# Kernel optimization log

Hardware: AMD Instinct MI355X
Metric: run time of the kernel (lower is better)

The kernel has to match this reference:

```python
import jax, jax.numpy as jnp
import numpy as np

N_NODES = 50000

def setup_inputs() -> dict:
    key = jax.random.key(0)
    k1, k2, k3, k4, k5 = jax.random.split(key, 5)
    E, F_IN, F_OUT = 1600000, 48, 48
    edge_feats = jax.random.normal(k1, (E, F_IN), dtype=jnp.float32)
    src = jax.random.randint(k2, (E,), 0, N_NODES, dtype=jnp.int64)
    dst = jax.random.randint(k3, (E,), 0, N_NODES, dtype=jnp.int64)
    # nn.Linear(in_feats, out_feats): weight [out, in], bias [out]
    lim = 1.0 / np.sqrt(F_IN)
    W = jax.random.uniform(k4, (F_OUT, F_IN), minval=-lim, maxval=lim, dtype=jnp.float32)
    b = jax.random.uniform(k5, (F_OUT,), minval=-lim, maxval=lim, dtype=jnp.float32)
    return {"edge_feats": edge_feats, "src": src, "dst": dst, "W": W, "b": b}

def reference(edge_feats, src, dst, W, b):
    # Step 1 (per-node loop in original): node h = mean of in-edge features
    deg = jax.ops.segment_sum(jnp.ones((edge_feats.shape[0],), edge_feats.dtype), dst, num_segments=N_NODES)
    node_h = jax.ops.segment_sum(edge_feats, dst, num_segments=N_NODES) / jnp.maximum(deg, 1.0)[:, None]
    # Step 2 (send/recv): node h' = sum over in-edges of src node h
    h2 = jax.ops.segment_sum(node_h[src], dst, num_segments=N_NODES)
    # Step 3 (edge_list loop): edge h = mean(h'[src], h'[dst])
    edge_h = 0.5 * (h2[src] + h2[dst])
    # Final linear on edge features
    return edge_h @ W.T + b
```

## Files before the change

### kernel.cpp

```cpp
#include <hip/hip_runtime.h>


constexpr int NN = 50000;
constexpr int F  = 48;
constexpr int F4 = F / 4;

typedef float    f32x4 __attribute__((ext_vector_type(4)));
typedef _Float16 f16x4 __attribute__((ext_vector_type(4)));

__global__ void k_zero(int* __restrict__ p, int n) {
    int i = blockIdx.x * blockDim.x + threadIdx.x;
    if (i < n) p[i] = 0;
}

__global__ void k_count(const int4* __restrict__ dst4, int* __restrict__ cnt, int E4) {
    int i = blockIdx.x * blockDim.x + threadIdx.x;
    if (i >= E4) return;
    int4 d = dst4[i];
    atomicAdd(&cnt[d.x], 1);
    atomicAdd(&cnt[d.y], 1);
    atomicAdd(&cnt[d.z], 1);
    atomicAdd(&cnt[d.w], 1);
}

__global__ __launch_bounds__(1024) void k_scan(
    const int4* __restrict__ cnt4, int4* __restrict__ rowptr4,
    int4* __restrict__ cursor4, int* __restrict__ rowptr, int n4, int n)
{
    __shared__ int wsum[16];
    __shared__ int carry_s;
    int t = threadIdx.x;
    int lane = t & 63, wid = t >> 6;
    if (t == 0) carry_s = 0;
    __syncthreads();
    for (int base = 0; base < n4; base += 1024) {
        int c0 = carry_s;
        int i4 = base + t;
        int4 v = (i4 < n4) ? cnt4[i4] : make_int4(0, 0, 0, 0);
        int tsum = v.x + v.y + v.z + v.w;
        int incl = tsum;
#pragma unroll
        for (int d = 1; d < 64; d <<= 1) {
            int u = __shfl_up(incl, d, 64);
            if (lane >= d) incl += u;
        }
        if (lane == 63) wsum[wid] = incl;
        __syncthreads();
        if (wid == 0) {
            int w = (lane < 16) ? wsum[lane] : 0;
            int wincl = w;
#pragma unroll
            for (int d = 1; d < 16; d <<= 1) {
                int u = __shfl_up(wincl, d, 64);
                if (lane >= d) wincl += u;
            }
            if (lane < 16) wsum[lane] = wincl - w;
        }
        __syncthreads();
        int excl = c0 + wsum[wid] + (incl - tsum);
        if (i4 < n4) {
            int p0 = excl, p1 = p0 + v.x, p2 = p1 + v.y, p3 = p2 + v.z;
            int4 r = make_int4(p0, p1, p2, p3);
            rowptr4[i4] = r;
            cursor4[i4] = r;
        }
        __syncthreads();
        if (t == 1023) carry_s = excl + tsum;
        __syncthreads();
    }
    if (t == 0) rowptr[n] = carry_s;
}

__global__ void k_fill(const int4* __restrict__ src4, const int4* __restrict__ dst4,
                       int* __restrict__ cursor, int2* __restrict__ csr_es, int E4) {
    int i = blockIdx.x * blockDim.x + threadIdx.x;
    if (i >= E4) return;
    int4 s = src4[i];
    int4 d = dst4[i];
    int e = i * 4;
    int p0 = atomicAdd(&cursor[d.x], 1);
    int p1 = atomicAdd(&cursor[d.y], 1);
    int p2 = atomicAdd(&cursor[d.z], 1);
    int p3 = atomicAdd(&cursor[d.w], 1);
    csr_es[p0] = make_int2(e + 0, s.x);
    csr_es[p1] = make_int2(e + 1, s.y);
    csr_es[p2] = make_int2(e + 2, s.z);
    csr_es[p3] = make_int2(e + 3, s.w);
}

__global__ __launch_bounds__(256) void k_node_h(
    const f32x4* __restrict__ ef4, const int2* __restrict__ csr_es,
    const int* __restrict__ rowptr, f16x4* __restrict__ nh16, int total)
{
    int idx = blockIdx.x * blockDim.x + threadIdx.x;
    if (idx >= total) return;
    int n = idx / F4;
    int q = idx - n * F4;
    int lo = rowptr[n], hi = rowptr[n + 1];
    f32x4 acc = (f32x4)(0.f);
    int j = lo;
    for (; j + 8 <= hi; j += 8) {
        int e0 = csr_es[j].x,     e1 = csr_es[j + 1].x;
        int e2 = csr_es[j + 2].x, e3 = csr_es[j + 3].x;
        int e4 = csr_es[j + 4].x, e5 = csr_es[j + 5].x;
        int e6 = csr_es[j + 6].x, e7 = csr_es[j + 7].x;
        f32x4 a0 = __builtin_nontemporal_load(&ef4[e0 * F4 + q]);
        f32x4 a1 = __builtin_nontemporal_load(&ef4[e1 * F4 + q]);
        f32x4 a2 = __builtin_nontemporal_load(&ef4[e2 * F4 + q]);
        f32x4 a3 = __builtin_nontemporal_load(&ef4[e3 * F4 + q]);
        f32x4 a4 = __builtin_nontemporal_load(&ef4[e4 * F4 + q]);
        f32x4 a5 = __builtin_nontemporal_load(&ef4[e5 * F4 + q]);
        f32x4 a6 = __builtin_nontemporal_load(&ef4[e6 * F4 + q]);
        f32x4 a7 = __builtin_nontemporal_load(&ef4[e7 * F4 + q]);
        acc += a0 + a1 + a2 + a3 + a4 + a5 + a6 + a7;
    }
    for (; j < hi; j++)
        acc += __builtin_nontemporal_load(&ef4[csr_es[j].x * F4 + q]);
    float inv = 1.0f / fmaxf((float)(hi - lo), 1.0f);
    acc *= inv;
    nh16[idx] = __builtin_convertvector(acc, f16x4);
}

__global__ __launch_bounds__(192) void k_h2lin(
    const f16x4* __restrict__ nh16, const int2* __restrict__ csr_es,
    const int* __restrict__ rowptr, const float* __restrict__ W,
    const float* __restrict__ b, f16x4* __restrict__ h2W16)
{
    __shared__ float h2s[16][F + 1];
    int t = threadIdx.x;
    int nl = t / F4, q = t - nl * F4;
    int node = blockIdx.x * 16 + nl;

    int lo = rowptr[node], hi = rowptr[node + 1];
    f32x4 acc = (f32x4)(0.f);
    int j = lo;
    for (; j + 4 <= hi; j += 4) {
        int s0 = csr_es[j].y,     s1 = csr_es[j + 1].y;
        int s2 = csr_es[j + 2].y, s3 = csr_es[j + 3].y;
        f32x4 a0 = __builtin_convertvector(nh16[s0 * F4 + q], f32x4);
        f32x4 a1 = __builtin_convertvector(nh16[s1 * F4 + q], f32x4);
        f32x4 a2 = __builtin_convertvector(nh16[s2 * F4 + q], f32x4);
        f32x4 a3 = __builtin_convertvector(nh16[s3 * F4 + q], f32x4);
        acc += a0 + a1 + a2 + a3;
    }
    for (; j < hi; j++)
        acc += __builtin_convertvector(nh16[csr_es[j].y * F4 + q], f32x4);

    h2s[nl][q * 4 + 0] = acc.x;
    h2s[nl][q * 4 + 1] = acc.y;
    h2s[nl][q * 4 + 2] = acc.z;
    h2s[nl][q * 4 + 3] = acc.w;
    __syncthreads();

    const float* row = h2s[nl];
    const float* W0 = W + (q * 4 + 0) * F;
    const float* W1 = W + (q * 4 + 1) * F;
    const float* W2 = W + (q * 4 + 2) * F;
    const float* W3 = W + (q * 4 + 3) * F;
    float o0 = 0.f, o1 = 0.f, o2 = 0.f, o3 = 0.f;
#pragma unroll
    for (int i = 0; i < F; i++) {
        float hv = row[i];
        o0 += hv * W0[i];
        o1 += hv * W1[i];
        o2 += hv * W2[i];
        o3 += hv * W3[i];
    }
    const f32x4* b4 = (const f32x4*)b;
    f32x4 r; r.x = o0; r.y = o1; r.z = o2; r.w = o3;
    r = 0.5f * r + 0.5f * b4[q];
    h2W16[node * F4 + q] = __builtin_convertvector(r, f16x4);
}

__global__ void k_edge_out(const int* __restrict__ src, const int* __restrict__ dst,
                           const f16x4* __restrict__ h2W16, f32x4* __restrict__ out4,
                           int total) {
    int idx = blockIdx.x * blockDim.x + threadIdx.x;
    if (idx >= total) return;
    int e = idx / F4;
    int q = idx - e * F4;
    f32x4 x = __builtin_convertvector(h2W16[src[e] * F4 + q], f32x4);
    f32x4 y = __builtin_convertvector(h2W16[dst[e] * F4 + q], f32x4);
    f32x4 r = x + y;
    __builtin_nontemporal_store(r, &out4[idx]);
}

extern "C" void kernel_launch(void* const* d_in, const int* in_sizes, int n_in,
                              void* d_out, int out_size, void* d_ws, size_t ws_size,
                              hipStream_t stream) {
    const float* ef  = (const float*)d_in[0];
    const int*   src = (const int*)d_in[1];
    const int*   dst = (const int*)d_in[2];
    const float* W   = (const float*)d_in[3];
    const float* b   = (const float*)d_in[4];
    float* out = (float*)d_out;
    const int E = in_sizes[1];

    _Float16* nh16  = (_Float16*)d_ws;
    _Float16* h2W16 = nh16 + NN * F;
    int2* csr_es    = (int2*)(h2W16 + NN * F);
    int* rowptr     = (int*)(csr_es + E);
    int* cursor     = rowptr + 50016;
    int* cnt        = cursor + 50016;

    const int totN4 = NN * F4;
    const int totE4 = E * F4;
    const int n4 = NN / 4;
    const int E4 = (E + 3) / 4;

    k_zero<<<(NN + 255) / 256, 256, 0, stream>>>(cnt, NN);
    k_count<<<(E4 + 255) / 256, 256, 0, stream>>>((const int4*)dst, cnt, E4);
    k_scan<<<1, 1024, 0, stream>>>((const int4*)cnt, (int4*)rowptr, (int4*)cursor,
                                   rowptr, n4, NN);
    k_fill<<<(E4 + 255) / 256, 256, 0, stream>>>(
        (const int4*)src, (const int4*)dst, cursor, csr_es, E4);
    k_node_h<<<(totN4 + 255) / 256, 256, 0, stream>>>(
        (const f32x4*)ef, csr_es, rowptr, (f16x4*)nh16, totN4);
    k_h2lin<<<NN / 16, 192, 0, stream>>>(
        (const f16x4*)nh16, csr_es, rowptr, W, b, (f16x4*)h2W16);
    k_edge_out<<<(totE4 + 255) / 256, 256, 0, stream>>>(
        src, dst, (const f16x4*)h2W16, (f32x4*)out, totE4);
}
```

Baseline: 464.0 us.

## Fuse all graph stages into one cooperative persistent kernel with grid syncs

Replaces the seven separate kernel launches with a single cooperative persistent kernel that runs each stage as a grid-stride loop separated by grid.sync. The single-block scan becomes a two-level scan spread across the grid. The h2/linear stage is split into an fp32 aggregation pass and a per-thread matvec that reads the full row from global memory instead of shared memory. The aim is to remove launch gaps and the serial single-block scan, at the cost of grid-wide barriers, a capped grid size (up to 1024 blocks) for the large edge loops, and extra global traffic for the new h2f buffer. The old multi-kernel path is kept as a fallback.

```diff
diff --git a/kernel.cpp b/kernel.cpp
--- a/kernel.cpp
+++ b/kernel.cpp
@@ -1,12 +1,208 @@
 #include <hip/hip_runtime.h>
-
-
-constexpr int NN = 50000;
-constexpr int F  = 48;
-constexpr int F4 = F / 4;
+#include <hip/hip_cooperative_groups.h>
+
+namespace cg = cooperative_groups;
+
+
+constexpr int NN   = 50000;
+constexpr int F    = 48;
+constexpr int F4   = F / 4;
+constexpr int NTHR = 256;
 
 typedef float    f32x4 __attribute__((ext_vector_type(4)));
 typedef _Float16 f16x4 __attribute__((ext_vector_type(4)));
+
+__global__ __launch_bounds__(NTHR, 4) void k_fused(
+    const f32x4* __restrict__ ef4,
+    const int4*  __restrict__ src4, const int4* __restrict__ dst4,
+    const int*   __restrict__ srcs, const int*  __restrict__ dsts,
+    const float* __restrict__ W,    const float* __restrict__ b,
+    f32x4* __restrict__ out4,
+    f16x4* __restrict__ nh16, f16x4* __restrict__ h2W16,
+    f32x4* __restrict__ h2f,
+    int2* __restrict__ csr_es, int* __restrict__ rowptr,
+    int* __restrict__ cursor,  int* __restrict__ cnt,
+    int* __restrict__ wavesum, int E)
+{
+    __shared__ int lws[4];
+    __shared__ int lwe[4];
+    cg::grid_group grid = cg::this_grid();
+
+    const int tid = blockIdx.x * NTHR + threadIdx.x;
+    const int NT  = gridDim.x * NTHR;
+    const int E4  = E >> 2;
+    const int totN4 = NN * F4;
+    const long totE4 = (long)E * F4;
+
+    for (int i = tid; i < NN; i += NT) cnt[i] = 0;
+    __threadfence();
+    grid.sync();
+
+    for (int i = tid; i < E4; i += NT) {
+        int4 d = dst4[i];
+        atomicAdd(&cnt[d.x], 1);
+        atomicAdd(&cnt[d.y], 1);
+        atomicAdd(&cnt[d.z], 1);
+        atomicAdd(&cnt[d.w], 1);
+    }
+    __threadfence();
+    grid.sync();
+
+    const int n4 = NN / 4;
+    const int gwid = tid >> 6, lane = tid & 63;
+    int4 v = make_int4(0, 0, 0, 0);
+    int tsum = 0, incl = 0;
+    if (tid < ((n4 + 63) & ~63)) {
+        if (tid < n4) {
+            v = ((const int4*)cnt)[tid];
+            tsum = v.x + v.y + v.z + v.w;
+        }
+        incl = tsum;
+#pragma unroll
+        for (int d = 1; d < 64; d <<= 1) {
+            int u = __shfl_up(incl, d, 64);
+            if (lane >= d) incl += u;
+        }
+        if (lane == 63) wavesum[gwid] = incl;
+    }
+    __threadfence();
+    grid.sync();
+
+    if (blockIdx.x == 0) {
+        int t = threadIdx.x;
+        int w = (t < 196) ? wavesum[t] : 0;
+        int wl = t & 63, wwid = t >> 6;
+        int winc = w;
+#pragma unroll
+        for (int d = 1; d < 64; d <<= 1) {
+            int u = __shfl_up(winc, d, 64);
+            if (wl >= d) winc += u;
+        }
+        if (wl == 63) lws[wwid] = winc;
+        __syncthreads();
+        if (t == 0) {
+            int run = 0;
+#pragma unroll
+            for (int k = 0; k < 4; k++) { lwe[k] = run; run += lws[k]; }
+            rowptr[NN] = E;
+        }
+        __syncthreads();
+        if (t < 196) wavesum[t] = lwe[wwid] + (winc - w);
+        __threadfence();
+    }
+    grid.sync();
+
+    if (tid < n4) {
+        int base = wavesum[gwid] + (incl - tsum);
+        int4 r;
+        r.x = base; r.y = base + v.x; r.z = r.y + v.y; r.w = r.z + v.z;
+        ((int4*)rowptr)[tid] = r;
+        ((int4*)cursor)[tid] = r;
+    }
+    __threadfence();
+    grid.sync();
+
+    for (int i = tid; i < E4; i += NT) {
+        int4 s = src4[i];
+        int4 d = dst4[i];
+        int e = i * 4;
+        int p0 = atomicAdd(&cursor[d.x], 1);
+        int p1 = atomicAdd(&cursor[d.y], 1);
+        int p2 = atomicAdd(&cursor[d.z], 1);
+        int p3 = atomicAdd(&cursor[d.w], 1);
+        csr_es[p0] = make_int2(e + 0, s.x);
+        csr_es[p1] = make_int2(e + 1, s.y);
+        csr_es[p2] = make_int2(e + 2, s.z);
+        csr_es[p3] = make_int2(e + 3, s.w);
+    }
+    __threadfence();
+    grid.sync();
+
+    for (int idx = tid; idx < totN4; idx += NT) {
+        int n = idx / F4, q = idx - n * F4;
+        int lo = rowptr[n], hi = rowptr[n + 1];
+        f32x4 acc = (f32x4)(0.f);
+        int j = lo;
+        for (; j + 8 <= hi; j += 8) {
+            int e0 = csr_es[j].x,     e1 = csr_es[j + 1].x;
+            int e2 = csr_es[j + 2].x, e3 = csr_es[j + 3].x;
+            int e4 = csr_es[j + 4].x, e5 = csr_es[j + 5].x;
+            int e6 = csr_es[j + 6].x, e7 = csr_es[j + 7].x;
+            f32x4 a0 = __builtin_nontemporal_load(&ef4[e0 * F4 + q]);
+            f32x4 a1 = __builtin_nontemporal_load(&ef4[e1 * F4 + q]);
+            f32x4 a2 = __builtin_nontemporal_load(&ef4[e2 * F4 + q]);
+            f32x4 a3 = __builtin_nontemporal_load(&ef4[e3 * F4 + q]);
+            f32x4 a4 = __builtin_nontemporal_load(&ef4[e4 * F4 + q]);
+            f32x4 a5 = __builtin_nontemporal_load(&ef4[e5 * F4 + q]);
+            f32x4 a6 = __builtin_nontemporal_load(&ef4[e6 * F4 + q]);
+            f32x4 a7 = __builtin_nontemporal_load(&ef4[e7 * F4 + q]);
+            acc += a0 + a1 + a2 + a3 + a4 + a5 + a6 + a7;
+        }
+        for (; j < hi; j++)
+            acc += __builtin_nontemporal_load(&ef4[csr_es[j].x * F4 + q]);
+        float inv = 1.0f / fmaxf((float)(hi - lo), 1.0f);
+        acc *= inv;
+        nh16[idx] = __builtin_convertvector(acc, f16x4);
+    }
+    __threadfence();
+    grid.sync();
+
+    for (int idx = tid; idx < totN4; idx += NT) {
+        int n = idx / F4, q = idx - n * F4;
+        int lo = rowptr[n], hi = rowptr[n + 1];
+        f32x4 acc = (f32x4)(0.f);
+        int j = lo;
+        for (; j + 4 <= hi; j += 4) {
+            int s0 = csr_es[j].y,     s1 = csr_es[j + 1].y;
+            int s2 = csr_es[j + 2].y, s3 = csr_es[j + 3].y;
+            f32x4 a0 = __builtin_convertvector(nh16[s0 * F4 + q], f32x4);
+            f32x4 a1 = __builtin_convertvector(nh16[s1 * F4 + q], f32x4);
+            f32x4 a2 = __builtin_convertvector(nh16[s2 * F4 + q], f32x4);
+            f32x4 a3 = __builtin_convertvector(nh16[s3 * F4 + q], f32x4);
+            acc += a0 + a1 + a2 + a3;
+        }
+        for (; j < hi; j++)
+            acc += __builtin_convertvector(nh16[csr_es[j].y * F4 + q], f32x4);
+        h2f[idx] = acc;
+    }
+    __threadfence();
+    grid.sync();
+
+    for (int idx = tid; idx < totN4; idx += NT) {
+        int n = idx / F4, q = idx - n * F4;
+        f32x4 rw[F4];
+#pragma unroll
+        for (int k = 0; k < F4; k++) rw[k] = h2f[n * F4 + k];
+        const float* row = (const float*)rw;
+        const float* W0 = W + (q * 4 + 0) * F;
+        const float* W1 = W + (q * 4 + 1) * F;
+        const float* W2 = W + (q * 4 + 2) * F;
+        const float* W3 = W + (q * 4 + 3) * F;
+        float o0 = 0.f, o1 = 0.f, o2 = 0.f, o3 = 0.f;
+#pragma unroll
+        for (int i = 0; i < F; i++) {
+            float hv = row[i];
+            o0 += hv * W0[i];
+            o1 += hv * W1[i];
+            o2 += hv * W2[i];
+            o3 += hv * W3[i];
+        }
+        const f32x4* b4 = (const f32x4*)b;
+        f32x4 r; r.x = o0; r.y = o1; r.z = o2; r.w = o3;
+        r = 0.5f * r + 0.5f * b4[q];
+        h2W16[idx] = __builtin_convertvector(r, f16x4);
+    }
+    __threadfence();
+    grid.sync();
+
+    for (long idx = tid; idx < totE4; idx += NT) {
+        int e = (int)(idx / F4), q = (int)(idx - (long)e * F4);
+        f32x4 x = __builtin_convertvector(h2W16[srcs[e] * F4 + q], f32x4);
+        f32x4 y = __builtin_convertvector(h2W16[dsts[e] * F4 + q], f32x4);
+        f32x4 r = x + y;
+        __builtin_nontemporal_store(r, &out4[idx]);
+    }
+}
 
 __global__ void k_zero(int* __restrict__ p, int n) {
     int i = blockIdx.x * blockDim.x + threadIdx.x;
@@ -194,30 +390,58 @@
     const float* W   = (const float*)d_in[3];
     const float* b   = (const float*)d_in[4];
     float* out = (float*)d_out;
-    const int E = in_sizes[1];
+    int E = in_sizes[1];
 
     _Float16* nh16  = (_Float16*)d_ws;
     _Float16* h2W16 = nh16 + NN * F;
-    int2* csr_es    = (int2*)(h2W16 + NN * F);
+    float* h2f      = (float*)(h2W16 + NN * F);
+    int2* csr_es    = (int2*)(h2f + NN * F);
     int* rowptr     = (int*)(csr_es + E);
     int* cursor     = rowptr + 50016;
     int* cnt        = cursor + 50016;
-
-    const int totN4 = NN * F4;
-    const int totE4 = E * F4;
-    const int n4 = NN / 4;
-    const int E4 = (E + 3) / 4;
-
-    k_zero<<<(NN + 255) / 256, 256, 0, stream>>>(cnt, NN);
-    k_count<<<(E4 + 255) / 256, 256, 0, stream>>>((const int4*)dst, cnt, E4);
-    k_scan<<<1, 1024, 0, stream>>>((const int4*)cnt, (int4*)rowptr, (int4*)cursor,
-                                   rowptr, n4, NN);
-    k_fill<<<(E4 + 255) / 256, 256, 0, stream>>>(
-        (const int4*)src, (const int4*)dst, cursor, csr_es, E4);
-    k_node_h<<<(totN4 + 255) / 256, 256, 0, stream>>>(
-        (const f32x4*)ef, csr_es, rowptr, (f16x4*)nh16, totN4);
-    k_h2lin<<<NN / 16, 192, 0, stream>>>(
-        (const f16x4*)nh16, csr_es, rowptr, W, b, (f16x4*)h2W16);
-    k_edge_out<<<(totE4 + 255) / 256, 256, 0, stream>>>(
-        src, dst, (const f16x4*)h2W16, (f32x4*)out, totE4);
-}
+    int* wavesum    = cnt + 50016;
+
+    const f32x4* ef4 = (const f32x4*)ef;
+    const int4* src4 = (const int4*)src;
+    const int4* dst4 = (const int4*)dst;
+    f32x4* out4 = (f32x4*)out;
+    f16x4* nh16v = (f16x4*)nh16;
+    f16x4* h2W16v = (f16x4*)h2W16;
+    f32x4* h2fv = (f32x4*)h2f;
+
+    int blocksPerCU = 0;
+    hipError_t qerr = hipOccupancyMaxActiveBlocksPerMultiprocessor(
+        &blocksPerCU, k_fused, NTHR, 0);
+    int nblk = (qerr == hipSuccess) ? blocksPerCU * 256 : 0;
+    if (nblk > 1024) nblk = 1024;
+
+    hipError_t lerr = hipErrorUnknown;
+    if (nblk >= 64) {
+        void* args[] = {
+            (void*)&ef4, (void*)&src4, (void*)&dst4, (void*)&src, (void*)&dst,
+            (void*)&W, (void*)&b, (void*)&out4,
+            (void*)&nh16v, (void*)&h2W16v, (void*)&h2fv,
+            (void*)&csr_es, (void*)&rowptr, (void*)&cursor, (void*)&cnt,
+            (void*)&wavesum, (void*)&E
+        };
+        lerr = hipLaunchCooperativeKernel((void*)k_fused, dim3(nblk), dim3(NTHR),
+                                          args, 0, stream);
+    }
+
+    if (lerr != hipSuccess) {
+        const int totN4 = NN * F4;
+        const int totE4 = E * F4;
+        const int n4 = NN / 4;
+        const int E4 = E / 4;
+        k_zero<<<(NN + 255) / 256, 256, 0, stream>>>(cnt, NN);
+        k_count<<<(E4 + 255) / 256, 256, 0, stream>>>(dst4, cnt, E4);
+        k_scan<<<1, 1024, 0, stream>>>((const int4*)cnt, (int4*)rowptr,
+                                       (int4*)cursor, rowptr, n4, NN);
+        k_fill<<<(E4 + 255) / 256, 256, 0, stream>>>(src4, dst4, cursor, csr_es, E4);
+        k_node_h<<<(totN4 + 255) / 256, 256, 0, stream>>>(
+            ef4, csr_es, rowptr, nh16v, totN4);
+        k_h2lin<<<NN / 16, 192, 0, stream>>>(nh16v, csr_es, rowptr, W, b, h2W16v);
+        k_edge_out<<<(totE4 + 255) / 256, 256, 0, stream>>>(
+            src, dst, h2W16v, out4, totE4);
+    }
+}
```

New measurement: 1.300 ms. 2.8x slower.
